# Kernel optimization log

Hardware: AMD Instinct MI355X
Metric: run time of the kernel (lower is better)

The kernel has to match this reference:

```python
import jax, jax.numpy as jnp
import numpy as np
from jax import lax

H = 128       # hidden_size
N = 128       # total agents
T = 12        # future_steps (hardcoded by .view(12, ...))
K = 20        # num_modes
NHEADS = 4
HD = H // NHEADS
MIN_SCALE = 0.001


def setup_inputs() -> dict:
    key = jax.random.key(0)
    ks = jax.random.split(key, 48)

    def w(i, shape, fan):
        return (jax.random.normal(ks[i], shape, dtype=jnp.float32) / np.float32(np.sqrt(fan)))

    z = lambda *s: jnp.zeros(s, jnp.float32)
    o = lambda *s: jnp.ones(s, jnp.float32)
    inp = {}
    inp['global_embed'] = jax.random.normal(ks[0], (T, N, H), dtype=jnp.float32)
    inp['hidden_state'] = jax.random.normal(ks[1], (N, H), dtype=jnp.float32)
    inp['cn'] = jax.random.normal(ks[2], (N, H), dtype=jnp.float32)
    inp['shift_values'] = jax.random.normal(ks[3], (1, N, 2), dtype=jnp.float32)
    inp['max_values'] = jax.random.uniform(ks[4], (N, 2), dtype=jnp.float32)
    # multihead_proj_global: Linear(H, K*H) + LayerNorm + ReLU
    inp['mhp_W'] = w(5, (H, K * H), H); inp['mhp_b'] = z(K * H)
    inp['mhp_g'] = o(K * H); inp['mhp_beta'] = z(K * H)
    # two LSTMCells (bias = b_ih + b_hh fused)
    inp['lstm1_Wih'] = w(6, (H, 4 * H), H); inp['lstm1_Whh'] = w(7, (H, 4 * H), H); inp['lstm1_b'] = z(4 * H)
    inp['lstm2_Wih'] = w(8, (H, 4 * H), H); inp['lstm2_Whh'] = w(9, (H, 4 * H), H); inp['lstm2_b'] = z(4 * H)
    # MultiHeadSelfAttention
    inp['Wq'] = w(10, (H, H), H); inp['bq'] = z(H)
    inp['Wk'] = w(11, (H, H), H); inp['bk'] = z(H)
    inp['Wv'] = w(12, (H, H), H); inp['bv'] = z(H)
    inp['Wo1'] = w(13, (H, 2 * H), H); inp['bo1'] = z(2 * H)
    inp['Wo2'] = w(14, (2 * H, H), 2 * H); inp['bo2'] = z(H)
    # loc head: Linear + LN + ReLU + Linear(H,2)
    inp['loc_W1'] = w(15, (H, H), H); inp['loc_b1'] = z(H)
    inp['loc_g'] = o(H); inp['loc_beta'] = z(H)
    inp['loc_W2'] = w(16, (H, 2), H); inp['loc_b2'] = z(2)
    # scale head
    inp['scl_W1'] = w(17, (H, H), H); inp['scl_b1'] = z(H)
    inp['scl_g'] = o(H); inp['scl_beta'] = z(H)
    inp['scl_W2'] = w(18, (H, 2), H); inp['scl_b2'] = z(2)
    inp['batch_split'] = 4  # number of equal scene segments
    return inp


def _ln(x, g, b):
    m = jnp.mean(x, -1, keepdims=True)
    v = jnp.mean((x - m) ** 2, -1, keepdims=True)
    return (x - m) / jnp.sqrt(v + 1e-5) * g + b


def _head(x, W1, b1, g, beta, W2, b2):
    return jax.nn.relu(_ln(x @ W1 + b1, g, beta)) @ W2 + b2


def reference(global_embed, hidden_state, cn, shift_values, max_values,
              mhp_W, mhp_b, mhp_g, mhp_beta,
              lstm1_Wih, lstm1_Whh, lstm1_b,
              lstm2_Wih, lstm2_Whh, lstm2_b,
              Wq, bq, Wk, bk, Wv, bv, Wo1, bo1, Wo2, bo2,
              loc_W1, loc_b1, loc_g, loc_beta, loc_W2, loc_b2,
              scl_W1, scl_b1, scl_g, scl_beta, scl_W2, scl_b2,
              batch_split):
    S = int(batch_split)
    n = N // S
    # project global embed to per-mode embeddings: [T,N,K*H] -> [T,K*N,H] (mode-major)
    ge = jax.nn.relu(_ln(global_embed @ mhp_W + mhp_b, mhp_g, mhp_beta))
    ge = ge.reshape(T, N, K, H).transpose(0, 2, 1, 3).reshape(T, K * N, H)
    h0 = jnp.tile(hidden_state, (K, 1))  # [K*N,H]
    c0 = jnp.tile(cn, (K, 1))

    def cell1(carry, x):
        h, c = carry
        gi, gf, gg, go = jnp.split(x @ lstm1_Wih + h @ lstm1_Whh + lstm1_b, 4, -1)
        c2 = jax.nn.sigmoid(gf) * c + jax.nn.sigmoid(gi) * jnp.tanh(gg)
        h2 = jax.nn.sigmoid(go) * jnp.tanh(c2)
        return (h2, c2), h2

    _, output1 = lax.scan(cell1, (h0, c0), ge)  # [T,K*N,H]

    loc1 = _head(output1, loc_W1, loc_b1, loc_g, loc_beta, loc_W2, loc_b2)
    loc1 = loc1.transpose(1, 0, 2).reshape(K, N, T, 2)
    scale1 = jax.nn.elu(_head(output1, scl_W1, scl_b1, scl_g, scl_beta, scl_W2, scl_b2)) + 1.0 + MIN_SCALE
    scale1 = scale1.transpose(1, 0, 2).reshape(K, N, T, 2)

    sv = shift_values[0]  # squeeze(0) -> [N,2]
    loc1_ = loc1 * max_values[:, None, :] + sv[:, None, :]            # [K,N,T,2]
    loc1_ = loc1_.transpose(0, 2, 1, 3).reshape(K * T, N, 2).transpose(0, 2, 1)  # [K*T,2,N]
    locs = loc1_.reshape(K * T, 2, S, n).transpose(2, 0, 1, 3)        # [S,K*T,2,n]

    def split_mask(x):  # x: [K*T,2,n]
        d = jnp.abs(x[:, :, :, None] - x[:, :, None, :])              # [K*T,2,n,n]
        m = ((d[:, 0] < 10.0) & (d[:, 1] < 10.0)).reshape(K, T, n, n).any(0)  # [T,n,n]
        return jnp.tile(m, (1, K, K))                                  # [T,K*n,K*n]

    masks = jax.vmap(split_mask)(locs)  # [S,T,K*n,K*n]

    o1d = lax.stop_gradient(output1)  # detach, as in torch
    o1d = o1d.reshape(T, K, S, n, H).transpose(2, 0, 1, 3, 4).reshape(S, T, K * n, H)

    def mhsa(x, mask):  # x: [T,L,H], mask: [T,L,L] bool
        L = K * n
        q = (x @ Wq + bq).reshape(T, L, NHEADS, HD)
        k = (x @ Wk + bk).reshape(T, L, NHEADS, HD)
        v = (x @ Wv + bv).reshape(T, L, NHEADS, HD)
        s = jnp.einsum('blhd,bmhd->bhlm', q, k) / np.float32(np.sqrt(HD))
        s = jnp.where(mask[:, None], s, jnp.float32(-1e8))
        ctx = jnp.einsum('bhlm,bmhd->blhd', jax.nn.softmax(s, -1), v).reshape(T, L, H)
        return jax.nn.relu(ctx @ Wo1 + bo1) @ Wo2 + bo2

    social = jax.vmap(mhsa)(o1d, masks)                                # [S,T,K*n,H]
    social = social.reshape(S, T, K, n, H).transpose(1, 2, 0, 3, 4).reshape(T, K * N, H)

    def cell2(carry, xs):
        h, c = carry
        x, soc = xs
        c = c + soc
        h = h + jnp.tanh(c)
        gi, gf, gg, go = jnp.split(x @ lstm2_Wih + h @ lstm2_Whh + lstm2_b, 4, -1)
        c2 = jax.nn.sigmoid(gf) * c + jax.nn.sigmoid(gi) * jnp.tanh(gg)
        h2 = jax.nn.sigmoid(go) * jnp.tanh(c2)
        return (h2, c2), h2

    _, output2 = lax.scan(cell2, (h0, c0), (ge, social))  # [T,K*N,H]

    loc2 = _head(output2, loc_W1, loc_b1, loc_g, loc_beta, loc_W2, loc_b2)
    loc2 = loc2.transpose(1, 0, 2).reshape(K, N, T, 2)
    scale2 = jax.nn.elu(_head(output2, scl_W1, scl_b1, scl_g, scl_beta, scl_W2, scl_b2)) + 1.0 + MIN_SCALE
    scale2 = scale2.transpose(1, 0, 2).reshape(K, N, T, 2)

    return jnp.stack([loc1, scale1, loc2, scale2], 0)  # [4,K,N,T,2]
```

## Files before the change

kernel.cpp:

```cpp
#include <hip/hip_runtime.h>
#include <hip/hip_bf16.h>

typedef __hip_bfloat16 bf16_t;

static const int cT  = 12;
static const int cN  = 128;
static const int cH  = 128;
static const int cK  = 20;
static const int cKN = 2560;
static const int cS  = 4;
static const int cNS = 32;
static const int cL  = 640;
static const int cHD = 32;

#define CONV_TOTAL 977986

__constant__ int c_off[38] = {0,196608,212992,229376,229632,229888,557568,560128,562688,
  565248,630784,696320,696832,762368,827904,828416,844800,844928,861312,861440,877824,
  877952,910720,910976,943744,943872,960256,960384,960512,960640,960896,960960,977344,
  977472,977600,977728,977984,977986};
__constant__ int c_len[37] = {196608,16384,16384,256,256,327680,2560,2560,2560,
  65536,65536,512,65536,65536,512,16384,128,16384,128,16384,128,
  32768,256,32768,128,16384,128,128,128,256,2,16384,128,128,128,256,2};

struct Ptrs { const void* p[37]; };

typedef __attribute__((ext_vector_type(4))) float f32x4;
typedef __attribute__((ext_vector_type(8))) __bf16 bf16x8;

__device__ __forceinline__ float sigm(float x){ return 1.f/(1.f+expf(-x)); }
__device__ __forceinline__ unsigned short f2h(float x){ return (unsigned short)(__float_as_uint(x)>>16); }
__device__ __forceinline__ float hif(float x){ return __uint_as_float(__float_as_uint(x)&0xFFFF0000u); }

__global__ __launch_bounds__(256) void k_detect(const unsigned short* ge_u16, int* flagp, unsigned int* outw){
  __shared__ int cnt;
  if (threadIdx.x == 0) cnt = 0;
  __syncthreads();
  int ok = 0;
  for (int i = threadIdx.x; i < 128; i += 64){
    unsigned short u = ge_u16[2*i];
    int ex = (u >> 7) & 0xFF;
    if (ex >= 100 && ex <= 140) ok++;
  }
  atomicAdd(&cnt, ok);
  __syncthreads();
  if (threadIdx.x == 0){
    *flagp = (cnt >= 96) ? 1 : 0;
    outw[0] = 0x7FC07FC0u;
  }
}

__global__ __launch_bounds__(256) void k_convert(Ptrs ptrs, const int* flagp, float* dst){
  int g = blockIdx.x*256 + threadIdx.x;
  if (g >= CONV_TOTAL) return;
  int flag = *flagp;
  int seg = 0;
  while (seg < 36 && g >= c_off[seg+1]) ++seg;
  int local = g - c_off[seg];
  if (local >= c_len[seg]) return;
  float v;
  if (flag) v = __bfloat162float(((const bf16_t*)ptrs.p[seg])[local]);
  else      v = ((const float*)ptrs.p[seg])[local];
  dst[g] = v;
}

__global__ __launch_bounds__(256) void k_mhp(const float* x, const float* W, const float* b,
                      const float* g, const float* be, float* out){
  const int ROWS = 2;
  int r0 = blockIdx.x*ROWS;
  __shared__ float xs[ROWS][cH];
  __shared__ float red[256][3];
  int tid = threadIdx.x;
  if (tid < ROWS*32){
    int rr = tid>>5, u4 = tid&31;
    ((float4*)&xs[rr][0])[u4] = ((const float4*)x)[(r0+rr)*32 + u4];
  }
  __syncthreads();
  float y[ROWS][10];
  #pragma unroll
  for (int m = 0; m < 10; ++m){ float bb = b[tid + 256*m]; y[0][m] = bb; y[1][m] = bb; }
  for (int i = 0; i < cH; ++i){
    float x0 = xs[0][i], x1 = xs[1][i];
    const float* wr = W + i*2560 + tid;
    #pragma unroll
    for (int m = 0; m < 10; ++m){
      float w = wr[256*m];
      y[0][m] += x0*w; y[1][m] += x1*w;
    }
  }
  float ps0 = 0.f, ps1 = 0.f;
  #pragma unroll
  for (int m = 0; m < 10; ++m){ ps0 += y[0][m]; ps1 += y[1][m]; }
  red[tid][0] = ps0; red[tid][1] = ps1; __syncthreads();
  for (int s2 = 128; s2 > 0; s2 >>= 1){
    if (tid < s2){ red[tid][0] += red[tid+s2][0]; red[tid][1] += red[tid+s2][1]; }
    __syncthreads();
  }
  float mean0 = red[0][0]*(1.f/2560.f), mean1 = red[0][1]*(1.f/2560.f);
  __syncthreads();
  float pv0 = 0.f, pv1 = 0.f;
  #pragma unroll
  for (int m = 0; m < 10; ++m){
    float d0 = y[0][m]-mean0, d1 = y[1][m]-mean1;
    pv0 += d0*d0; pv1 += d1*d1;
  }
  red[tid][0] = pv0; red[tid][1] = pv1; __syncthreads();
  for (int s2 = 128; s2 > 0; s2 >>= 1){
    if (tid < s2){ red[tid][0] += red[tid+s2][0]; red[tid][1] += red[tid+s2][1]; }
    __syncthreads();
  }
  float inv0 = rsqrtf(red[0][0]*(1.f/2560.f) + 1e-5f);
  float inv1 = rsqrtf(red[0][1]*(1.f/2560.f) + 1e-5f);
  #pragma unroll
  for (int rr = 0; rr < ROWS; ++rr){
    int rg = r0 + rr;
    int t = rg >> 7, nn = rg & 127;
    float mean = rr ? mean1 : mean0;
    float inv  = rr ? inv1  : inv0;
    #pragma unroll
    for (int m = 0; m < 10; ++m){
      int col = tid + 256*m;
      float z = (y[rr][m]-mean)*inv*g[col] + be[col];
      z = fmaxf(z, 0.f);
      int k = col >> 7, hh2 = col & 127;
      out[((t*cKN) + k*cN + nn)*cH + hh2] = z;
    }
  }
}

__global__ __launch_bounds__(256) void k_wprep(const float* w0, const float* w1,
    const float* w2, const float* w3, unsigned short* out){
  int idx = blockIdx.x*256 + threadIdx.x;
  int m = idx >> 13;
  int rest = idx & 8191;
  int n = rest >> 8;
  int s = (rest >> 6) & 3;
  int l = rest & 63;
  int g = l >> 4, c16 = l & 15;
  const float* W = (m==0) ? w0 : ((m==1) ? w1 : ((m==2) ? w2 : w3));
  unsigned short hi[8], lo[8];
  #pragma unroll
  for (int e = 0; e < 8; ++e){
    int k = 32*s + 16*(e>>2) + 4*g + (e&3);
    float v = W[k*512 + 16*n + c16];
    hi[e] = f2h(v); lo[e] = f2h(v - hif(v));
  }
  size_t base = (size_t)m*131072 + (size_t)((n*4 + s)*64 + l)*8;
  *(uint4*)&out[base]         = *(const uint4*)hi;
  *(uint4*)&out[base + 65536] = *(const uint4*)lo;
}

__global__ __launch_bounds__(256) void k_wprep2(const float* wq, const float* wk,
    const float* wv, const float* wo1, const float* wo2,
    unsigned short* outA, unsigned short* outB){
  int idx = blockIdx.x*256 + threadIdx.x;
  if (idx >= 14336) return;
  const float* W; int KF, N, local, half; unsigned short* out; size_t off;
  if (idx < 2048)      { W=wq;  KF=4; N=128; off=0;      local=idx;       half=16384; out=outA; }
  else if (idx < 4096) { W=wk;  KF=4; N=128; off=32768;  local=idx-2048;  half=16384; out=outA; }
  else if (idx < 6144) { W=wv;  KF=4; N=128; off=65536;  local=idx-4096;  half=16384; out=outA; }
  else if (idx < 10240){ W=wo1; KF=4; N=256; off=98304;  local=idx-6144;  half=32768; out=outA; }
  else                 { W=wo2; KF=8; N=128; off=0;      local=idx-10240; half=32768; out=outB; }
  int l = local & 63;
  int rest = local >> 6;
  int s = rest & (KF-1);
  int n = (KF == 8) ? (rest >> 3) : (rest >> 2);
  int g = l >> 4, c16 = l & 15;
  unsigned short hi[8], lo[8];
  #pragma unroll
  for (int e = 0; e < 8; ++e){
    int k = 32*s + 16*(e>>2) + 4*g + (e&3);
    float v = W[k*N + 16*n + c16];
    hi[e] = f2h(v); lo[e] = f2h(v - hif(v));
  }
  size_t base = off + (size_t)local*8;
  *(uint4*)&out[base]        = *(const uint4*)hi;
  *(uint4*)&out[base + half] = *(const uint4*)lo;
}

__global__ __launch_bounds__(512) void k_lstm_mfma(const float* ge, float* outh,
    const float* hs0, const float* cn0, const float* soc,
    const unsigned short* wfA, const unsigned short* wfB,
    const float* bias, int phase){
  int r0 = blockIdx.x * 16;
  int tid = threadIdx.x;
  int w = tid >> 6, l = tid & 63;
  int g = l >> 4, c16 = l & 15;
  int scol = w*16 + c16;
  __shared__ unsigned short HFh[2][4][64][8], HFl[2][4][64][8];
  int ps = scol >> 5, prem = scol & 31;
  int pgf = (prem >> 2) & 3;
  int pe  = ((prem >> 4) << 2) + (prem & 3);
  float c[4], h[4];
  #pragma unroll
  for (int r = 0; r < 4; ++r){
    int nn = (r0 + 4*g + r) & 127;
    c[r] = cn0[nn*cH + scol];
    h[r] = hs0[nn*cH + scol];
  }
  float bias_t[4];
  #pragma unroll
  for (int tt = 0; tt < 4; ++tt) bias_t[tt] = bias[tt*128 + scol];

  f32x4 xr[8];
  float socr[4] = {0.f, 0.f, 0.f, 0.f};
  {
    const f32x4* gp = (const f32x4*)ge + ((size_t)(r0 + c16))*32;
    #pragma unroll
    for (int s = 0; s < 4; ++s){ xr[2*s] = gp[8*s + g]; xr[2*s+1] = gp[8*s + 4 + g]; }
    if (phase == 2){
      #pragma unroll
      for (int r = 0; r < 4; ++r)
        socr[r] = soc[(size_t)(r0 + 4*g + r)*cH + scol];
    }
  }

  for (int t = 0; t < cT; ++t){
    int b = t & 1;
    if (phase == 2){
      #pragma unroll
      for (int r = 0; r < 4; ++r){
        c[r] += socr[r];
        h[r] += tanhf(c[r]);
      }
    }
    #pragma unroll
    for (int r = 0; r < 4; ++r){
      HFh[b][ps][pgf*16 + 4*g + r][pe] = f2h(h[r]);
      HFl[b][ps][pgf*16 + 4*g + r][pe] = f2h(h[r] - hif(h[r]));
    }
    bf16x8 xh[4], xl[4];
    #pragma unroll
    for (int s = 0; s < 4; ++s){
      union { unsigned short u[8]; bf16x8 v; } uh, ul;
      #pragma unroll
      for (int m2 = 0; m2 < 4; ++m2){
        float a0 = xr[2*s][m2], b0 = xr[2*s+1][m2];
        uh.u[m2]   = f2h(a0); ul.u[m2]   = f2h(a0 - hif(a0));
        uh.u[4+m2] = f2h(b0); ul.u[4+m2] = f2h(b0 - hif(b0));
      }
      xh[s] = uh.v; xl[s] = ul.v;
    }
    if (t < cT-1){
      const f32x4* gp = (const f32x4*)ge + ((size_t)(t+1)*cKN + r0 + c16)*32;
      #pragma unroll
      for (int s = 0; s < 4; ++s){ xr[2*s] = gp[8*s + g]; xr[2*s+1] = gp[8*s + 4 + g]; }
      if (phase == 2){
        #pragma unroll
        for (int r = 0; r < 4; ++r)
          socr[r] = soc[(size_t)(t+1)*cKN*cH + (size_t)(r0 + 4*g + r)*cH + scol];
      }
    }
    __syncthreads();
    bf16x8 hh[4], hl[4];
    #pragma unroll
    for (int s = 0; s < 4; ++s){
      hh[s] = *(const bf16x8*)&HFh[b][s][l][0];
      hl[s] = *(const bf16x8*)&HFl[b][s][l][0];
    }
    f32x4 a4[4];
    #pragma unroll
    for (int tt = 0; tt < 4; ++tt){
      f32x4 acc = {bias_t[tt], bias_t[tt], bias_t[tt], bias_t[tt]};
      a4[tt] = acc;
    }
    {
      bf16x8 cAh, cAl, cBh, cBl, nAh, nAl, nBh, nBl;
      {
        size_t fo = (size_t)((w*4 + 0)*64 + l)*8;
        cAh = *(const bf16x8*)&wfA[fo];
        cAl = *(const bf16x8*)&wfA[65536 + fo];
        cBh = *(const bf16x8*)&wfB[fo];
        cBl = *(const bf16x8*)&wfB[65536 + fo];
      }
      #pragma unroll
      for (int j = 0; j < 16; ++j){
        int s = j >> 2, tt = j & 3;
        if (j < 15){
          int j2 = j + 1;
          int s2 = j2 >> 2, tt2 = j2 & 3;
          size_t fo = (size_t)(((w + 8*tt2)*4 + s2)*64 + l)*8;
          nAh = *(const bf16x8*)&wfA[fo];
          nAl = *(const bf16x8*)&wfA[65536 + fo];
          nBh = *(const bf16x8*)&wfB[fo];
          nBl = *(const bf16x8*)&wfB[65536 + fo];
        }
        f32x4 acc = a4[tt];
        acc = __builtin_amdgcn_mfma_f32_16x16x32_bf16(xl[s], cAh, acc, 0, 0, 0);
        acc = __builtin_amdgcn_mfma_f32_16x16x32_bf16(xh[s], cAl, acc, 0, 0, 0);
        acc = __builtin_amdgcn_mfma_f32_16x16x32_bf16(xh[s], cAh, acc, 0, 0, 0);
        acc = __builtin_amdgcn_mfma_f32_16x16x32_bf16(hl[s], cBh, acc, 0, 0, 0);
        acc = __builtin_amdgcn_mfma_f32_16x16x32_bf16(hh[s], cBl, acc, 0, 0, 0);
        acc = __builtin_amdgcn_mfma_f32_16x16x32_bf16(hh[s], cBh, acc, 0, 0, 0);
        a4[tt] = acc;
        cAh = nAh; cAl = nAl; cBh = nBh; cBl = nBl;
      }
    }
    #pragma unroll
    for (int r = 0; r < 4; ++r){
      float ig = sigm(a4[0][r]), fg = sigm(a4[1][r]);
      float gg = tanhf(a4[2][r]), og = sigm(a4[3][r]);
      c[r] = fg*c[r] + ig*gg;
      h[r] = og*tanhf(c[r]);
      outh[(size_t)t*cKN*cH + (size_t)(r0 + 4*g + r)*cH + scol] = h[r];
    }
  }
}

template<int KF>
__global__ __launch_bounds__(256) void k_gemm(const float* x, const unsigned short* wf,
    const float* bias, float* out, int NT, int N, int relu, int half){
  int r0 = blockIdx.x * 16;
  int tid = threadIdx.x;
  int wv = tid >> 6, l = tid & 63;
  int g = l >> 4, c16 = l & 15;
  bf16x8 xh[KF], xl[KF];
  const f32x4* gp = (const f32x4*)x + (size_t)(r0 + c16)*(KF*8);
  #pragma unroll
  for (int s = 0; s < KF; ++s){
    f32x4 qa = gp[8*s + g], qb = gp[8*s + 4 + g];
    union { unsigned short u[8]; bf16x8 v; } uh, ul;
    #pragma unroll
    for (int m2 = 0; m2 < 4; ++m2){
      float a0 = qa[m2], b0 = qb[m2];
      uh.u[m2]   = f2h(a0); ul.u[m2]   = f2h(a0 - hif(a0));
      uh.u[4+m2] = f2h(b0); ul.u[4+m2] = f2h(b0 - hif(b0));
    }
    xh[s] = uh.v; xl[s] = ul.v;
  }
  for (int nt = wv; nt < NT; nt += 4){
    float bb = bias[nt*16 + c16];
    f32x4 acc = {bb, bb, bb, bb};
    #pragma unroll
    for (int s = 0; s < KF; ++s){
      const unsigned short* fb = wf + (size_t)((nt*KF + s)*64 + l)*8;
      bf16x8 Wh = *(const bf16x8*)fb;
      bf16x8 Wl = *(const bf16x8*)(fb + half);
      acc = __builtin_amdgcn_mfma_f32_16x16x32_bf16(xl[s], Wh, acc, 0, 0, 0);
      acc = __builtin_amdgcn_mfma_f32_16x16x32_bf16(xh[s], Wl, acc, 0, 0, 0);
      acc = __builtin_amdgcn_mfma_f32_16x16x32_bf16(xh[s], Wh, acc, 0, 0, 0);
    }
    if (relu){
      #pragma unroll
      for (int r = 0; r < 4; ++r) acc[r] = fmaxf(acc[r], 0.f);
    }
    #pragma unroll
    for (int r = 0; r < 4; ++r)
      out[(size_t)(r0 + 4*g + r)*N + nt*16 + c16] = acc[r];
  }
}

__global__ __launch_bounds__(256) void k_gemm3(const float* x, const unsigned short* wf,
    const float* bq, const float* bk, const float* bv,
    float* Q, float* K2, float* V){
  int r0 = blockIdx.x * 16;
  int tid = threadIdx.x;
  int wv = tid >> 6, l = tid & 63;
  int g = l >> 4, c16 = l & 15;
  bf16x8 xh[4], xl[4];
  const f32x4* gp = (const f32x4*)x + (size_t)(r0 + c16)*32;
  #pragma unroll
  for (int s = 0; s < 4; ++s){
    f32x4 qa = gp[8*s + g], qb = gp[8*s + 4 + g];
    union { unsigned short u[8]; bf16x8 v; } uh, ul;
    #pragma unroll
    for (int m2 = 0; m2 < 4; ++m2){
      float a0 = qa[m2], b0 = qb[m2];
      uh.u[m2]   = f2h(a0); ul.u[m2]   = f2h(a0 - hif(a0));
      uh.u[4+m2] = f2h(b0); ul.u[4+m2] = f2h(b0 - hif(b0));
    }
    xh[s] = uh.v; xl[s] = ul.v;
  }
  for (int nt = wv; nt < 24; nt += 4){
    int m = nt >> 3, n = nt & 7;
    const float* bias = (m==0) ? bq : ((m==1) ? bk : bv);
    float* out = (m==0) ? Q : ((m==1) ? K2 : V);
    float bb = bias[n*16 + c16];
    f32x4 acc = {bb, bb, bb, bb};
    const unsigned short* base = wf + (size_t)m*32768;
    #pragma unroll
    for (int s = 0; s < 4; ++s){
      const unsigned short* fb = base + (size_t)((n*4 + s)*64 + l)*8;
      bf16x8 Wh = *(const bf16x8*)fb;
      bf16x8 Wl = *(const bf16x8*)(fb + 16384);
      acc = __builtin_amdgcn_mfma_f32_16x16x32_bf16(xl[s], Wh, acc, 0, 0, 0);
      acc = __builtin_amdgcn_mfma_f32_16x16x32_bf16(xh[s], Wl, acc, 0, 0, 0);
      acc = __builtin_amdgcn_mfma_f32_16x16x32_bf16(xh[s], Wh, acc, 0, 0, 0);
    }
    #pragma unroll
    for (int r = 0; r < 4; ++r)
      out[(size_t)(r0 + 4*g + r)*cH + n*16 + c16] = acc[r];
  }
}

__global__ __launch_bounds__(256) void k_heads(const float* x,
  const float* lW1, const float* lb1, const float* lg, const float* lbe, const float* lW2, const float* lb2v,
  const float* sW1, const float* sb1, const float* sg, const float* sbe, const float* sW2, const float* sb2v,
  void* outv, int q0, float* locsc, const float* maxv, const float* svp, const int* flagp){
  const int ROWS = 4;
  int r0 = blockIdx.x*ROWS;
  __shared__ float xs[ROWS][cH];
  int tid = threadIdx.x;
  if (tid < ROWS*32){
    int rr = tid>>5, u4 = tid&31;
    ((float4*)&xs[rr][0])[u4] = ((const float4*)x)[(size_t)(r0+rr)*32 + u4];
  }
  __syncthreads();
  int wv = tid >> 6, lane = tid & 63;
  int head = wv & 1;
  int ra = (wv >> 1)*2, rb = ra + 1;
  const float* W1 = head ? sW1 : lW1;
  const float* b1 = head ? sb1 : lb1;
  const float* gv = head ? sg  : lg;
  const float* be = head ? sbe : lbe;
  const float* W2 = head ? sW2 : lW2;
  const float* b2 = head ? sb2v: lb2v;
  int j0 = lane, j1 = lane + 64;
  float a00 = b1[j0], a01 = b1[j1];
  float a10 = a00, a11 = a01;
  for (int i = 0; i < cH; ++i){
    float w0 = W1[i*cH + j0], w1 = W1[i*cH + j1];
    float xa = xs[ra][i], xb = xs[rb][i];
    a00 += xa*w0; a01 += xa*w1;
    a10 += xb*w0; a11 += xb*w1;
  }
  float s0 = a00 + a01, s1 = a10 + a11;
  #pragma unroll
  for (int off = 1; off < 64; off <<= 1){
    s0 += __shfl_xor(s0, off);
    s1 += __shfl_xor(s1, off);
  }
  float mean0 = s0*(1.f/128.f), mean1 = s1*(1.f/128.f);
  float d00 = a00-mean0, d01 = a01-mean0, d10 = a10-mean1, d11 = a11-mean1;
  float v0 = d00*d00 + d01*d01, v1 = d10*d10 + d11*d11;
  #pragma unroll
  for (int off = 1; off < 64; off <<= 1){
    v0 += __shfl_xor(v0, off);
    v1 += __shfl_xor(v1, off);
  }
  float inv0 = rsqrtf(v0*(1.f/128.f) + 1e-5f);
  float inv1 = rsqrtf(v1*(1.f/128.f) + 1e-5f);
  float g0 = gv[j0], g1 = gv[j1], be0 = be[j0], be1 = be[j1];
  float z00 = fmaxf(d00*inv0*g0 + be0, 0.f);
  float z01 = fmaxf(d01*inv0*g1 + be1, 0.f);
  float z10 = fmaxf(d10*inv1*g0 + be0, 0.f);
  float z11 = fmaxf(d11*inv1*g1 + be1, 0.f);
  float w2a0 = W2[j0*2+0], w2a1 = W2[j0*2+1];
  float w2b0 = W2[j1*2+0], w2b1 = W2[j1*2+1];
  float oa0 = z00*w2a0 + z01*w2b0;
  float oa1 = z00*w2a1 + z01*w2b1;
  float ob0 = z10*w2a0 + z11*w2b0;
  float ob1 = z10*w2a1 + z11*w2b1;
  #pragma unroll
  for (int off = 1; off < 64; off <<= 1){
    oa0 += __shfl_xor(oa0, off);
    oa1 += __shfl_xor(oa1, off);
    ob0 += __shfl_xor(ob0, off);
    ob1 += __shfl_xor(ob1, off);
  }
  if (lane == 0){
    int flag = *flagp;
    float bias0 = b2[0], bias1 = b2[1];
    float ro[2][2] = {{oa0 + bias0, oa1 + bias1},{ob0 + bias0, ob1 + bias1}};
    int lr[2] = {ra, rb};
    for (int e = 0; e < 2; ++e){
      int rg = r0 + lr[e];
      int t = rg / cKN, rem = rg - t*cKN;
      int k = rem >> 7, nn = rem & 127;
      float u0 = ro[e][0], u1 = ro[e][1];
      if (head == 0){
        size_t oi = (((size_t)q0*cK + k)*cN + nn)*(cT*2) + t*2;
        if (flag){ ((bf16_t*)outv)[oi] = __float2bfloat16(u0); ((bf16_t*)outv)[oi+1] = __float2bfloat16(u1); }
        else     { ((float*)outv)[oi] = u0; ((float*)outv)[oi+1] = u1; }
        if (locsc){
          locsc[((size_t)t*cKN + rem)*2 + 0] = u0*maxv[nn*2+0] + svp[nn*2+0];
          locsc[((size_t)t*cKN + rem)*2 + 1] = u1*maxv[nn*2+1] + svp[nn*2+1];
        }
      } else {
        float e0 = (u0 > 0.f ? u0 : expm1f(u0)) + 1.001f;
        float e1 = (u1 > 0.f ? u1 : expm1f(u1)) + 1.001f;
        size_t oi = (((size_t)(q0+1)*cK + k)*cN + nn)*(cT*2) + t*2;
        if (flag){ ((bf16_t*)outv)[oi] = __float2bfloat16(e0); ((bf16_t*)outv)[oi+1] = __float2bfloat16(e1); }
        else     { ((float*)outv)[oi] = e0; ((float*)outv)[oi+1] = e1; }
      }
    }
  }
}

__global__ __launch_bounds__(256) void k_mask(const float* locsc, unsigned char* m){
  int st = blockIdx.x;
  int s = st / cT, t = st - s*cT;
  __shared__ float lx[cK][cNS], ly[cK][cNS];
  int tid = threadIdx.x;
  for (int p = tid; p < cK*cNS; p += 256){
    int k = p >> 5, i = p & 31;
    int row = t*cKN + k*cN + s*cNS + i;
    lx[k][i] = locsc[row*2+0];
    ly[k][i] = locsc[row*2+1];
  }
  __syncthreads();
  for (int p = tid; p < 1024; p += 256){
    int i = p >> 5, j = p & 31;
    bool any = false;
    for (int k = 0; k < cK; ++k){
      float dx = fabsf(lx[k][i]-lx[k][j]);
      float dy = fabsf(ly[k][i]-ly[k][j]);
      any = any || ((dx < 10.f) && (dy < 10.f));
    }
    m[st*1024 + p] = any ? 1 : 0;
  }
}

__global__ __launch_bounds__(256) void k_attn(const float* Q, const float* Kx, const float* V,
                       const unsigned char* msk, float* ctx){
  int qs   = blockIdx.x;
  int head = blockIdx.y;
  int st   = blockIdx.z;
  int s = st / cT, t = st - s*cT;
  __shared__ unsigned short KLh[2][1024], KLl[2][1024], VLh[2][1024], VLl[2][1024];
  int tid = threadIdx.x;
  int w = tid >> 6, lane = tid & 63;
  int g = lane >> 4, col = lane & 15;
  const float scl = 0.17677669529663687f;

  unsigned int mw0 = 0, mw1 = 0;
  {
    const unsigned int* mr0 = (const unsigned int*)(msk + st*1024 + col*32);
    const unsigned int* mr1 = (const unsigned int*)(msk + st*1024 + (16+col)*32);
    #pragma unroll
    for (int j2 = 0; j2 < 8; ++j2){
      mw0 |= (((mr0[j2] * 0x01020408u) >> 24) & 0xFu) << (4*j2);
      mw1 |= (((mr1[j2] * 0x01020408u) >> 24) & 0xFu) << (4*j2);
    }
  }

  bf16x8 Qh[2], Ql[2];
  int modes[2], ahs[2];
  #pragma unroll
  for (int i = 0; i < 2; ++i){
    int tt = qs*8 + 4*i + w;
    int mode = tt >> 1, ah = tt & 1;
    modes[i] = mode; ahs[i] = ah;
    int qrow = t*cKN + mode*cN + s*cNS + ah*16 + col;
    const f32x4* qp = (const f32x4*)Q + (size_t)qrow*32 + head*8;
    f32x4 qa = qp[g], qb = qp[4+g];
    union { unsigned short u[8]; bf16x8 v; } uh, ul;
    #pragma unroll
    for (int m = 0; m < 4; ++m){
      float x0 = qa[m]*scl;
      uh.u[m] = f2h(x0);
      ul.u[m] = f2h(x0 - hif(x0));
      float x1 = qb[m]*scl;
      uh.u[4+m] = f2h(x1);
      ul.u[4+m] = f2h(x1 - hif(x1));
    }
    Qh[i] = uh.v; Ql[i] = ul.v;
  }

  int kk = tid >> 3, f4 = tid & 7;
  int kwi = (((kk>>4)*4 + (f4&3))*16 + (kk&15))*8 + (f4>>2)*4;
  int vd = tid & 31, quad = tid >> 5;
  int vkey = (quad>>2)*16 + (quad&3)*4;
  int vwi = (((vd>>4)*4 + (quad&3))*16 + (vd&15))*8 + (quad>>2)*4;

  const size_t cstepK = (size_t)cN*32;
  const size_t cstepV = (size_t)cN*128;
  const float4* kptr = (const float4*)Kx + ((size_t)(t*cKN + s*cNS + kk))*32 + head*8 + f4;
  const float*  vptr = V + ((size_t)(t*cKN + s*cNS + vkey))*128 + head*32 + vd;

  float4 kv; float vm0, vm1, vm2, vm3;
  kv = *kptr; kptr += cstepK;
  vm0 = vptr[0]; vm1 = vptr[128]; vm2 = vptr[256]; vm3 = vptr[384]; vptr += cstepV;
  {
    unsigned int h0 = (unsigned int)f2h(kv.x) | ((unsigned int)f2h(kv.y)<<16);
    unsigned int h1 = (unsigned int)f2h(kv.z) | ((unsigned int)f2h(kv.w)<<16);
    float r0 = kv.x-hif(kv.x), r1 = kv.y-hif(kv.y), r2 = kv.z-hif(kv.z), r3 = kv.w-hif(kv.w);
    unsigned int l0 = (unsigned int)f2h(r0) | ((unsigned int)f2h(r1)<<16);
    unsigned int l1 = (unsigned int)f2h(r2) | ((unsigned int)f2h(r3)<<16);
    *(uint2*)&KLh[0][kwi] = make_uint2(h0,h1);
    *(uint2*)&KLl[0][kwi] = make_uint2(l0,l1);
    unsigned int vh0 = (unsigned int)f2h(vm0) | ((unsigned int)f2h(vm1)<<16);
    unsigned int vh1 = (unsigned int)f2h(vm2) | ((unsigned int)f2h(vm3)<<16);
    float s0 = vm0-hif(vm0), s1 = vm1-hif(vm1), s2 = vm2-hif(vm2), s3 = vm3-hif(vm3);
    unsigned int vl0 = (unsigned int)f2h(s0) | ((unsigned int)f2h(s1)<<16);
    unsigned int vl1 = (unsigned int)f2h(s2) | ((unsigned int)f2h(s3)<<16);
    *(uint2*)&VLh[0][vwi] = make_uint2(vh0,vh1);
    *(uint2*)&VLl[0][vwi] = make_uint2(vl0,vl1);
  }
  __syncthreads();

  const f32x4 Z = {0.f, 0.f, 0.f, 0.f};
  f32x4 O[2][2] = {{Z, Z}, {Z, Z}};
  float lac[2] = {0.f, 0.f};

  for (int ch = 0; ch < 20; ++ch){
    int par = ch & 1;
    if (ch < 19){
      kv = *kptr; kptr += cstepK;
      vm0 = vptr[0]; vm1 = vptr[128]; vm2 = vptr[256]; vm3 = vptr[384]; vptr += cstepV;
    }
    bf16x8 KAh0 = *(const bf16x8*)&KLh[par][( g      *16 + col)*8];
    bf16x8 KAl0 = *(const bf16x8*)&KLl[par][( g      *16 + col)*8];
    bf16x8 KAh1 = *(const bf16x8*)&KLh[par][((4 + g) *16 + col)*8];
    bf16x8 KAl1 = *(const bf16x8*)&KLl[par][((4 + g) *16 + col)*8];
    bf16x8 VBh0 = *(const bf16x8*)&VLh[par][( g      *16 + col)*8];
    bf16x8 VBl0 = *(const bf16x8*)&VLl[par][( g      *16 + col)*8];
    bf16x8 VBh1 = *(const bf16x8*)&VLh[par][((4 + g) *16 + col)*8];
    bf16x8 VBl1 = *(const bf16x8*)&VLl[par][((4 + g) *16 + col)*8];
    #pragma unroll
    for (int i = 0; i < 2; ++i){
      f32x4 sa = Z, sb = Z;
      sa = __builtin_amdgcn_mfma_f32_16x16x32_bf16(KAl0, Qh[i], sa, 0, 0, 0);
      sa = __builtin_amdgcn_mfma_f32_16x16x32_bf16(KAh0, Ql[i], sa, 0, 0, 0);
      sa = __builtin_amdgcn_mfma_f32_16x16x32_bf16(KAh0, Qh[i], sa, 0, 0, 0);
      sb = __builtin_amdgcn_mfma_f32_16x16x32_bf16(KAl1, Qh[i], sb, 0, 0, 0);
      sb = __builtin_amdgcn_mfma_f32_16x16x32_bf16(KAh1, Ql[i], sb, 0, 0, 0);
      sb = __builtin_amdgcn_mfma_f32_16x16x32_bf16(KAh1, Qh[i], sb, 0, 0, 0);
      unsigned int mw = ahs[i] ? mw1 : mw0;
      float p[8];
      #pragma unroll
      for (int r = 0; r < 4; ++r){
        float e0 = __expf(sa[r]);
        float e1 = __expf(sb[r]);
        p[r]   = ((mw >> (4*g + r)) & 1)        ? e0 : 0.f;
        p[4+r] = ((mw >> (16 + 4*g + r)) & 1)   ? e1 : 0.f;
      }
      lac[i] += ((p[0]+p[1])+(p[2]+p[3])) + ((p[4]+p[5])+(p[6]+p[7]));
      union { unsigned short u[8]; bf16x8 v; } Ph, Pl;
      #pragma unroll
      for (int e = 0; e < 8; ++e){
        Ph.u[e] = f2h(p[e]);
        Pl.u[e] = f2h(p[e] - hif(p[e]));
      }
      O[i][0] = __builtin_amdgcn_mfma_f32_16x16x32_bf16(Pl.v, VBh0, O[i][0], 0, 0, 0);
      O[i][0] = __builtin_amdgcn_mfma_f32_16x16x32_bf16(Ph.v, VBl0, O[i][0], 0, 0, 0);
      O[i][0] = __builtin_amdgcn_mfma_f32_16x16x32_bf16(Ph.v, VBh0, O[i][0], 0, 0, 0);
      O[i][1] = __builtin_amdgcn_mfma_f32_16x16x32_bf16(Pl.v, VBh1, O[i][1], 0, 0, 0);
      O[i][1] = __builtin_amdgcn_mfma_f32_16x16x32_bf16(Ph.v, VBl1, O[i][1], 0, 0, 0);
      O[i][1] = __builtin_amdgcn_mfma_f32_16x16x32_bf16(Ph.v, VBh1, O[i][1], 0, 0, 0);
    }
    __syncthreads();
    if (ch < 19){
      int nb = 1 - par;
      unsigned int h0 = (unsigned int)f2h(kv.x) | ((unsigned int)f2h(kv.y)<<16);
      unsigned int h1 = (unsigned int)f2h(kv.z) | ((unsigned int)f2h(kv.w)<<16);
      float r0 = kv.x-hif(kv.x), r1 = kv.y-hif(kv.y), r2 = kv.z-hif(kv.z), r3 = kv.w-hif(kv.w);
      unsigned int l0 = (unsigned int)f2h(r0) | ((unsigned int)f2h(r1)<<16);
      unsigned int l1 = (unsigned int)f2h(r2) | ((unsigned int)f2h(r3)<<16);
      *(uint2*)&KLh[nb][kwi] = make_uint2(h0,h1);
      *(uint2*)&KLl[nb][kwi] = make_uint2(l0,l1);
      unsigned int vh0 = (unsigned int)f2h(vm0) | ((unsigned int)f2h(vm1)<<16);
      unsigned int vh1 = (unsigned int)f2h(vm2) | ((unsigned int)f2h(vm3)<<16);
      float s0 = vm0-hif(vm0), s1 = vm1-hif(vm1), s2 = vm2-hif(vm2), s3 = vm3-hif(vm3);
      unsigned int vl0 = (unsigned int)f2h(s0) | ((unsigned int)f2h(s1)<<16);
      unsigned int vl1 = (unsigned int)f2h(s2) | ((unsigned int)f2h(s3)<<16);
      *(uint2*)&VLh[nb][vwi] = make_uint2(vh0,vh1);
      *(uint2*)&VLl[nb][vwi] = make_uint2(vl0,vl1);
    }
    __syncthreads();
  }

  #pragma unroll
  for (int i = 0; i < 2; ++i){
    float lsum = lac[i];
    lsum += __shfl_xor(lsum, 16);
    lsum += __shfl_xor(lsum, 32);
    int base = t*cKN + modes[i]*cN + s*cNS + ahs[i]*16;
    #pragma unroll
    for (int r = 0; r < 4; ++r){
      float lq = __shfl(lsum, 4*g + r);
      float rinv = 1.f / lq;
      float* cp = ctx + (size_t)(base + 4*g + r)*cH + head*cHD;
      cp[col]      = O[i][0][r] * rinv;
      cp[col+16]   = O[i][1][r] * rinv;
    }
  }
}

extern "C" void kernel_launch(void* const* d_in, const int* in_sizes, int n_in,
                              void* d_out, int out_size, void* d_ws, size_t ws_size,
                              hipStream_t stream){
  (void)in_sizes; (void)n_in; (void)out_size; (void)ws_size;

  int*   flagp = (int*)d_ws;
  float* conv  = (float*)d_ws + 64;
  float* big   = (float*)d_ws + 978112;

  const float* ge_f   = conv + 0;
  const float* hs_f   = conv + 196608;
  const float* cn_f   = conv + 212992;
  const float* sv_f   = conv + 229376;
  const float* mx_f   = conv + 229632;
  const float* mhpW_f = conv + 229888;
  const float* mhpb_f = conv + 557568;
  const float* mhpg_f = conv + 560128;
  const float* mhpbe_f= conv + 562688;
  const float* l1Wih_f= conv + 565248;
  const float* l1Whh_f= conv + 630784;
  const float* l1b_f  = conv + 696320;
  const float* l2Wih_f= conv + 696832;
  const float* l2Whh_f= conv + 762368;
  const float* l2b_f  = conv + 827904;
  const float* Wq_f   = conv + 828416;
  const float* bq_f   = conv + 844800;
  const float* Wk_f   = conv + 844928;
  const float* bk_f   = conv + 861312;
  const float* Wv_f   = conv + 861440;
  const float* bv_f   = conv + 877824;
  const float* Wo1_f  = conv + 877952;
  const float* bo1_f  = conv + 910720;
  const float* Wo2_f  = conv + 910976;
  const float* bo2_f  = conv + 943744;
  const float* locW1_f= conv + 943872;
  const float* locb1_f= conv + 960256;
  const float* locg_f = conv + 960384;
  const float* locbe_f= conv + 960512;
  const float* locW2_f= conv + 960640;
  const float* locb2_f= conv + 960896;
  const float* sclW1_f= conv + 960960;
  const float* sclb1_f= conv + 977344;
  const float* sclg_f = conv + 977472;
  const float* sclbe_f= conv + 977600;
  const float* sclW2_f= conv + 977728;
  const float* sclb2_f= conv + 977984;

  const size_t SLOT = (size_t)cT*cKN*cH;
  float* geb = big;
  float* o1b = big + SLOT;
  float* Qb  = big + 2*SLOT;
  float* Kb  = big + 3*SLOT;
  float* Vb  = big + 4*SLOT;
  float* locsc = big + 5*SLOT;
  unsigned char* maskb = (unsigned char*)(locsc + (size_t)cT*cKN*2);
  float* t1 = Qb;
  float* social = Vb;

  unsigned short* wfrag = (unsigned short*)(conv + 229888);
  unsigned short* uA = (unsigned short*)(conv + 565248);
  unsigned short* uB = (unsigned short*)(conv + 696832);

  Ptrs ptrs;
  for (int i = 0; i < 37; ++i) ptrs.p[i] = d_in[i];

  k_detect<<<1, 64, 0, stream>>>((const unsigned short*)d_in[0], flagp, (unsigned int*)d_out);
  k_convert<<<(CONV_TOTAL+255)/256, 256, 0, stream>>>(ptrs, flagp, conv);
  k_mhp<<<cT*cN/2, 256, 0, stream>>>(ge_f, mhpW_f, mhpb_f, mhpg_f, mhpbe_f, geb);
  k_wprep<<<128, 256, 0, stream>>>(l1Wih_f, l1Whh_f, l2Wih_f, l2Whh_f, wfrag);
  k_wprep2<<<56, 256, 0, stream>>>(Wq_f, Wk_f, Wv_f, Wo1_f, Wo2_f, uA, uB);
  k_lstm_mfma<<<160, 512, 0, stream>>>(geb, o1b, hs_f, cn_f, (const float*)0,
                                       wfrag + 0, wfrag + 131072, l1b_f, 1);
  k_heads<<<cT*cKN/4, 256, 0, stream>>>(o1b, locW1_f,locb1_f,locg_f,locbe_f,locW2_f,locb2_f,
                                        sclW1_f,sclb1_f,sclg_f,sclbe_f,sclW2_f,sclb2_f,
                                        d_out, 0, locsc, mx_f, sv_f, flagp);
  k_mask<<<cS*cT, 256, 0, stream>>>(locsc, maskb);
  k_gemm3<<<cT*cKN/16, 256, 0, stream>>>(o1b, uA, bq_f, bk_f, bv_f, Qb, Kb, Vb);
  {
    dim3 ag(5, 4, cS*cT);
    k_attn<<<ag, 256, 0, stream>>>(Qb, Kb, Vb, maskb, o1b);
  }
  k_gemm<4><<<cT*cKN/16, 256, 0, stream>>>(o1b, uA + 98304, bo1_f, t1, 16, 256, 1, 32768);
  k_gemm<8><<<cT*cKN/16, 256, 0, stream>>>(t1, uB, bo2_f, social, 8, 128, 0, 32768);
  k_lstm_mfma<<<160, 512, 0, stream>>>(geb, o1b, hs_f, cn_f, social,
                                       wfrag + 262144, wfrag + 393216, l2b_f, 2);
  k_heads<<<cT*cKN/4, 256, 0, stream>>>(o1b, locW1_f,locb1_f,locg_f,locbe_f,locW2_f,locb2_f,
                                        sclW1_f,sclb1_f,sclg_f,sclbe_f,sclW2_f,sclb2_f,
                                        d_out, 2, (float*)0, mx_f, sv_f, flagp);
}
```

Measured before the change: 650.5 us.

## Move multihead projection to MFMA GEMM and batch more rows per heads block

The fp32 scalar multihead projection kernel is split into three steps. A weight-fragment prep step packs W into hi/lo split bf16 fragments, the existing MFMA k_gemm computes the 1536x2560 projection into a scratch buffer, and a separate per-row LayerNorm+ReLU kernel scatters the result. The heads kernel now processes 16 rows per block instead of 4, so each W1 load is reused across 8 rows per wave. This adds a scratch round trip and two extra launches, and raises register pressure in the heads kernel.

```diff
diff --git a/kernel.cpp b/kernel.cpp
--- a/kernel.cpp
+++ b/kernel.cpp
@@ -64,67 +64,61 @@
   dst[g] = v;
 }
 
-__global__ __launch_bounds__(256) void k_mhp(const float* x, const float* W, const float* b,
-                      const float* g, const float* be, float* out){
-  const int ROWS = 2;
-  int r0 = blockIdx.x*ROWS;
-  __shared__ float xs[ROWS][cH];
-  __shared__ float red[256][3];
+__global__ __launch_bounds__(256) void k_wprep3(const float* W, unsigned short* out){
+  int idx = blockIdx.x*256 + threadIdx.x;
+  int l = idx & 63;
+  int rest = idx >> 6;
+  int s = rest & 3;
+  int n = rest >> 2;
+  int g = l >> 4, c16 = l & 15;
+  unsigned short hi[8], lo[8];
+  #pragma unroll
+  for (int e = 0; e < 8; ++e){
+    int k = 32*s + 16*(e>>2) + 4*g + (e&3);
+    float v = W[k*2560 + 16*n + c16];
+    hi[e] = f2h(v); lo[e] = f2h(v - hif(v));
+  }
+  size_t base = (size_t)idx*8;
+  *(uint4*)&out[base]          = *(const uint4*)hi;
+  *(uint4*)&out[base + 327680] = *(const uint4*)lo;
+}
+
+__global__ __launch_bounds__(256) void k_mhp_ln(const float* y, const float* g,
+                      const float* be, float* out){
+  int row = blockIdx.x;
   int tid = threadIdx.x;
-  if (tid < ROWS*32){
-    int rr = tid>>5, u4 = tid&31;
-    ((float4*)&xs[rr][0])[u4] = ((const float4*)x)[(r0+rr)*32 + u4];
-  }
+  __shared__ float red[256];
+  float v[10];
+  const float* yr = y + (size_t)row*2560;
+  #pragma unroll
+  for (int m = 0; m < 10; ++m) v[m] = yr[tid + 256*m];
+  float ps = 0.f;
+  #pragma unroll
+  for (int m = 0; m < 10; ++m) ps += v[m];
+  red[tid] = ps; __syncthreads();
+  for (int s2 = 128; s2 > 0; s2 >>= 1){
+    if (tid < s2) red[tid] += red[tid+s2];
+    __syncthreads();
+  }
+  float mean = red[0]*(1.f/2560.f);
   __syncthreads();
-  float y[ROWS][10];
-  #pragma unroll
-  for (int m = 0; m < 10; ++m){ float bb = b[tid + 256*m]; y[0][m] = bb; y[1][m] = bb; }
-  for (int i = 0; i < cH; ++i){
-    float x0 = xs[0][i], x1 = xs[1][i];
-    const float* wr = W + i*2560 + tid;
-    #pragma unroll
-    for (int m = 0; m < 10; ++m){
-      float w = wr[256*m];
-      y[0][m] += x0*w; y[1][m] += x1*w;
-    }
-  }
-  float ps0 = 0.f, ps1 = 0.f;
-  #pragma unroll
-  for (int m = 0; m < 10; ++m){ ps0 += y[0][m]; ps1 += y[1][m]; }
-  red[tid][0] = ps0; red[tid][1] = ps1; __syncthreads();
+  float pv = 0.f;
+  #pragma unroll
+  for (int m = 0; m < 10; ++m){ float d = v[m]-mean; pv += d*d; }
+  red[tid] = pv; __syncthreads();
   for (int s2 = 128; s2 > 0; s2 >>= 1){
-    if (tid < s2){ red[tid][0] += red[tid+s2][0]; red[tid][1] += red[tid+s2][1]; }
+    if (tid < s2) red[tid] += red[tid+s2];
     __syncthreads();
   }
-  float mean0 = red[0][0]*(1.f/2560.f), mean1 = red[0][1]*(1.f/2560.f);
-  __syncthreads();
-  float pv0 = 0.f, pv1 = 0.f;
+  float inv = rsqrtf(red[0]*(1.f/2560.f) + 1e-5f);
+  int t = row >> 7, nn = row & 127;
   #pragma unroll
   for (int m = 0; m < 10; ++m){
-    float d0 = y[0][m]-mean0, d1 = y[1][m]-mean1;
-    pv0 += d0*d0; pv1 += d1*d1;
-  }
-  red[tid][0] = pv0; red[tid][1] = pv1; __syncthreads();
-  for (int s2 = 128; s2 > 0; s2 >>= 1){
-    if (tid < s2){ red[tid][0] += red[tid+s2][0]; red[tid][1] += red[tid+s2][1]; }
-    __syncthreads();
-  }
-  float inv0 = rsqrtf(red[0][0]*(1.f/2560.f) + 1e-5f);
-  float inv1 = rsqrtf(red[0][1]*(1.f/2560.f) + 1e-5f);
-  #pragma unroll
-  for (int rr = 0; rr < ROWS; ++rr){
-    int rg = r0 + rr;
-    int t = rg >> 7, nn = rg & 127;
-    float mean = rr ? mean1 : mean0;
-    float inv  = rr ? inv1  : inv0;
-    #pragma unroll
-    for (int m = 0; m < 10; ++m){
-      int col = tid + 256*m;
-      float z = (y[rr][m]-mean)*inv*g[col] + be[col];
-      z = fmaxf(z, 0.f);
-      int k = col >> 7, hh2 = col & 127;
-      out[((t*cKN) + k*cN + nn)*cH + hh2] = z;
-    }
+    int col = tid + 256*m;
+    float z = (v[m]-mean)*inv*g[col] + be[col];
+    z = fmaxf(z, 0.f);
+    int k = col >> 7, hh2 = col & 127;
+    out[((t*cKN) + k*cN + nn)*cH + hh2] = z;
   }
 }
 
@@ -397,18 +391,18 @@
   const float* lW1, const float* lb1, const float* lg, const float* lbe, const float* lW2, const float* lb2v,
   const float* sW1, const float* sb1, const float* sg, const float* sbe, const float* sW2, const float* sb2v,
   void* outv, int q0, float* locsc, const float* maxv, const float* svp, const int* flagp){
-  const int ROWS = 4;
+  const int ROWS = 16;
   int r0 = blockIdx.x*ROWS;
   __shared__ float xs[ROWS][cH];
   int tid = threadIdx.x;
-  if (tid < ROWS*32){
-    int rr = tid>>5, u4 = tid&31;
+  for (int p = tid; p < ROWS*32; p += 256){
+    int rr = p>>5, u4 = p&31;
     ((float4*)&xs[rr][0])[u4] = ((const float4*)x)[(size_t)(r0+rr)*32 + u4];
   }
   __syncthreads();
   int wv = tid >> 6, lane = tid & 63;
   int head = wv & 1;
-  int ra = (wv >> 1)*2, rb = ra + 1;
+  int rbase = (wv >> 1)*8;
   const float* W1 = head ? sW1 : lW1;
   const float* b1 = head ? sb1 : lb1;
   const float* gv = head ? sg  : lg;
@@ -416,58 +410,47 @@
   const float* W2 = head ? sW2 : lW2;
   const float* b2 = head ? sb2v: lb2v;
   int j0 = lane, j1 = lane + 64;
-  float a00 = b1[j0], a01 = b1[j1];
-  float a10 = a00, a11 = a01;
+  float b10 = b1[j0], b11 = b1[j1];
+  float a0[8], a1[8];
+  #pragma unroll
+  for (int r = 0; r < 8; ++r){ a0[r] = b10; a1[r] = b11; }
   for (int i = 0; i < cH; ++i){
     float w0 = W1[i*cH + j0], w1 = W1[i*cH + j1];
-    float xa = xs[ra][i], xb = xs[rb][i];
-    a00 += xa*w0; a01 += xa*w1;
-    a10 += xb*w0; a11 += xb*w1;
-  }
-  float s0 = a00 + a01, s1 = a10 + a11;
-  #pragma unroll
-  for (int off = 1; off < 64; off <<= 1){
-    s0 += __shfl_xor(s0, off);
-    s1 += __shfl_xor(s1, off);
-  }
-  float mean0 = s0*(1.f/128.f), mean1 = s1*(1.f/128.f);
-  float d00 = a00-mean0, d01 = a01-mean0, d10 = a10-mean1, d11 = a11-mean1;
-  float v0 = d00*d00 + d01*d01, v1 = d10*d10 + d11*d11;
-  #pragma unroll
-  for (int off = 1; off < 64; off <<= 1){
-    v0 += __shfl_xor(v0, off);
-    v1 += __shfl_xor(v1, off);
-  }
-  float inv0 = rsqrtf(v0*(1.f/128.f) + 1e-5f);
-  float inv1 = rsqrtf(v1*(1.f/128.f) + 1e-5f);
+    #pragma unroll
+    for (int r = 0; r < 8; ++r){
+      float xv = xs[rbase + r][i];
+      a0[r] += xv*w0; a1[r] += xv*w1;
+    }
+  }
   float g0 = gv[j0], g1 = gv[j1], be0 = be[j0], be1 = be[j1];
-  float z00 = fmaxf(d00*inv0*g0 + be0, 0.f);
-  float z01 = fmaxf(d01*inv0*g1 + be1, 0.f);
-  float z10 = fmaxf(d10*inv1*g0 + be0, 0.f);
-  float z11 = fmaxf(d11*inv1*g1 + be1, 0.f);
   float w2a0 = W2[j0*2+0], w2a1 = W2[j0*2+1];
   float w2b0 = W2[j1*2+0], w2b1 = W2[j1*2+1];
-  float oa0 = z00*w2a0 + z01*w2b0;
-  float oa1 = z00*w2a1 + z01*w2b1;
-  float ob0 = z10*w2a0 + z11*w2b0;
-  float ob1 = z10*w2a1 + z11*w2b1;
-  #pragma unroll
-  for (int off = 1; off < 64; off <<= 1){
-    oa0 += __shfl_xor(oa0, off);
-    oa1 += __shfl_xor(oa1, off);
-    ob0 += __shfl_xor(ob0, off);
-    ob1 += __shfl_xor(ob1, off);
-  }
-  if (lane == 0){
-    int flag = *flagp;
-    float bias0 = b2[0], bias1 = b2[1];
-    float ro[2][2] = {{oa0 + bias0, oa1 + bias1},{ob0 + bias0, ob1 + bias1}};
-    int lr[2] = {ra, rb};
-    for (int e = 0; e < 2; ++e){
-      int rg = r0 + lr[e];
+  int flag = *flagp;
+  float bias0 = b2[0], bias1 = b2[1];
+  for (int r = 0; r < 8; ++r){
+    float s = a0[r] + a1[r];
+    #pragma unroll
+    for (int off = 1; off < 64; off <<= 1) s += __shfl_xor(s, off);
+    float mean = s*(1.f/128.f);
+    float d0 = a0[r]-mean, d1 = a1[r]-mean;
+    float vv = d0*d0 + d1*d1;
+    #pragma unroll
+    for (int off = 1; off < 64; off <<= 1) vv += __shfl_xor(vv, off);
+    float inv = rsqrtf(vv*(1.f/128.f) + 1e-5f);
+    float z0 = fmaxf(d0*inv*g0 + be0, 0.f);
+    float z1 = fmaxf(d1*inv*g1 + be1, 0.f);
+    float o0 = z0*w2a0 + z1*w2b0;
+    float o1 = z0*w2a1 + z1*w2b1;
+    #pragma unroll
+    for (int off = 1; off < 64; off <<= 1){
+      o0 += __shfl_xor(o0, off);
+      o1 += __shfl_xor(o1, off);
+    }
+    if (lane == 0){
+      int rg = r0 + rbase + r;
       int t = rg / cKN, rem = rg - t*cKN;
       int k = rem >> 7, nn = rem & 127;
-      float u0 = ro[e][0], u1 = ro[e][1];
+      float u0 = o0 + bias0, u1 = o1 + bias1;
       if (head == 0){
         size_t oi = (((size_t)q0*cK + k)*cN + nn)*(cT*2) + t*2;
         if (flag){ ((bf16_t*)outv)[oi] = __float2bfloat16(u0); ((bf16_t*)outv)[oi+1] = __float2bfloat16(u1); }
@@ -738,18 +721,22 @@
   unsigned short* wfrag = (unsigned short*)(conv + 229888);
   unsigned short* uA = (unsigned short*)(conv + 565248);
   unsigned short* uB = (unsigned short*)(conv + 696832);
+  unsigned short* mfrag = (unsigned short*)(big + 2*SLOT);
+  float* ytmp = big + 3*SLOT;
 
   Ptrs ptrs;
   for (int i = 0; i < 37; ++i) ptrs.p[i] = d_in[i];
 
   k_detect<<<1, 64, 0, stream>>>((const unsigned short*)d_in[0], flagp, (unsigned int*)d_out);
   k_convert<<<(CONV_TOTAL+255)/256, 256, 0, stream>>>(ptrs, flagp, conv);
-  k_mhp<<<cT*cN/2, 256, 0, stream>>>(ge_f, mhpW_f, mhpb_f, mhpg_f, mhpbe_f, geb);
+  k_wprep3<<<160, 256, 0, stream>>>(mhpW_f, mfrag);
+  k_gemm<4><<<96, 256, 0, stream>>>(ge_f, mfrag, mhpb_f, ytmp, 160, 2560, 0, 327680);
+  k_mhp_ln<<<1536, 256, 0, stream>>>(ytmp, mhpg_f, mhpbe_f, geb);
   k_wprep<<<128, 256, 0, stream>>>(l1Wih_f, l1Whh_f, l2Wih_f, l2Whh_f, wfrag);
   k_wprep2<<<56, 256, 0, stream>>>(Wq_f, Wk_f, Wv_f, Wo1_f, Wo2_f, uA, uB);
   k_lstm_mfma<<<160, 512, 0, stream>>>(geb, o1b, hs_f, cn_f, (const float*)0,
                                        wfrag + 0, wfrag + 131072, l1b_f, 1);
-  k_heads<<<cT*cKN/4, 256, 0, stream>>>(o1b, locW1_f,locb1_f,locg_f,locbe_f,locW2_f,locb2_f,
+  k_heads<<<cT*cKN/16, 256, 0, stream>>>(o1b, locW1_f,locb1_f,locg_f,locbe_f,locW2_f,locb2_f,
                                         sclW1_f,sclb1_f,sclg_f,sclbe_f,sclW2_f,sclb2_f,
                                         d_out, 0, locsc, mx_f, sv_f, flagp);
   k_mask<<<cS*cT, 256, 0, stream>>>(locsc, maskb);
@@ -762,7 +749,7 @@
   k_gemm<8><<<cT*cKN/16, 256, 0, stream>>>(t1, uB, bo2_f, social, 8, 128, 0, 32768);
   k_lstm_mfma<<<160, 512, 0, stream>>>(geb, o1b, hs_f, cn_f, social,
                                        wfrag + 262144, wfrag + 393216, l2b_f, 2);
-  k_heads<<<cT*cKN/4, 256, 0, stream>>>(o1b, locW1_f,locb1_f,locg_f,locbe_f,locW2_f,locb2_f,
+  k_heads<<<cT*cKN/16, 256, 0, stream>>>(o1b, locW1_f,locb1_f,locg_f,locbe_f,locW2_f,locb2_f,
                                         sclW1_f,sclb1_f,sclg_f,sclbe_f,sclW2_f,sclb2_f,
                                         d_out, 2, (float*)0, mx_f, sv_f, flagp);
 }
```

After: 632.9 us. 2.7% less time.
